# Kernel tuning notes

Measured on AMD Instinct MI355X. Metric: run time of the kernel, lower is better.

Reference implementation:

```python
import jax, jax.numpy as jnp
import numpy as np

N = 4096      # num_nodes (single graph; batch is all-zeros in the original when absent)
CIN = 1024    # in_channels
H = 1024      # hidden_channels
COUT = 512    # out_channels
R = 10        # nodevec rank (hardcoded in the module)
BN_EPS = 1e-5


def setup_inputs() -> dict:
    key = jax.random.key(0)
    ks = jax.random.split(key, 8)
    w = lambda k, shp: jax.random.normal(k, shp, dtype=jnp.float32) * 0.02
    return {
        "x": jax.random.normal(ks[0], (N, CIN), dtype=jnp.float32),
        "w_map": w(ks[1], (CIN, H)),
        "b_map": jnp.zeros((H,), jnp.float32),
        "nv1": jax.random.normal(ks[2], (N, R), dtype=jnp.float32),
        "nv2": jax.random.normal(ks[3], (R, N), dtype=jnp.float32),
        "w1": w(ks[4], (H, H)),
        "b1": jnp.zeros((H,), jnp.float32),
        "w2": w(ks[5], (H, COUT)),
        "b2": jnp.zeros((COUT,), jnp.float32),
        "bn1_g": jnp.ones((H,), jnp.float32),
        "bn1_b": jnp.zeros((H,), jnp.float32),
        "bn1_m": jnp.zeros((H,), jnp.float32),
        "bn1_v": jnp.ones((H,), jnp.float32),
        "bn2_g": jnp.ones((COUT,), jnp.float32),
        "bn2_b": jnp.zeros((COUT,), jnp.float32),
        "bn2_m": jnp.zeros((COUT,), jnp.float32),
        "bn2_v": jnp.ones((COUT,), jnp.float32),
        "w_attn": w(ks[6], (COUT, 1)),
        "b_attn": jnp.zeros((1,), jnp.float32),
    }


def _batchnorm_eval(h, g, b, m, v):
    # BatchNorm1d in eval mode: running stats
    return (h - m) * jax.lax.rsqrt(v + BN_EPS) * g + b


def reference(x, w_map, b_map, nv1, nv2, w1, b1, w2, b2,
              bn1_g, bn1_b, bn1_m, bn1_v, bn2_g, bn2_b, bn2_m, bn2_v,
              w_attn, b_attn):
    # feature mapping
    xm = jax.nn.relu(x @ w_map + b_map)                       # [N, H]
    # adaptive adjacency: softmax(relu(nv1 @ nv2), dim=1) -> strictly positive,
    # so nonzero() yields the fully dense edge list; we keep it dense.
    adp = jax.nn.softmax(jax.nn.relu(nv1 @ nv2), axis=1)      # [N, N]
    # gcn_norm (PyG GCNConv default): add unit self-loops, normalize by
    # column-degree^-1/2 on both sides.
    A = adp + jnp.eye(N, dtype=adp.dtype)                      # [N, N]
    deg = jnp.sum(A, axis=0)                                   # column sums (target degree)
    dinv = jnp.where(deg > 0, jax.lax.rsqrt(deg), 0.0)
    An = (dinv[:, None] * A) * dinv[None, :]                   # D^-1/2 A D^-1/2
    # GCNConv: out_i = sum_j An[j, i] * (x W)_j + bias  =>  An^T @ (X W) + b
    h = jax.nn.relu(An.T @ (xm @ w1) + b1)                     # conv1 + relu
    h = _batchnorm_eval(h, bn1_g, bn1_b, bn1_m, bn1_v)         # bn1 (dropout off in eval)
    h = jax.nn.relu(An.T @ (h @ w2) + b2)                      # conv2 + relu
    h = _batchnorm_eval(h, bn2_g, bn2_b, bn2_m, bn2_v)         # bn2
    # global_mean_pool with batch == zeros -> single-graph mean
    pooled = jnp.mean(h, axis=0, keepdims=True)                # [1, COUT]
    attn = jax.nn.sigmoid(pooled @ w_attn + b_attn)            # [1, 1]
    return pooled * attn                                       # [1, COUT]
```

## Files before the change

kernel.cpp:

```cpp
#include <hip/hip_runtime.h>

#define NN 4096
#define R_RANK 10

typedef __bf16 bf16x8 __attribute__((ext_vector_type(8)));
typedef float floatx4 __attribute__((ext_vector_type(4)));

__device__ __forceinline__ unsigned short f2bf(float f) {
    union { float f; unsigned int u; } v; v.f = f;
    unsigned int r = v.u + 0x7FFFu + ((v.u >> 16) & 1u);
    return (unsigned short)(r >> 16);
}
__device__ __forceinline__ void gll16(const void* g, void* l) {
    __builtin_amdgcn_global_load_lds(
        (const __attribute__((address_space(1))) unsigned int*)g,
        (__attribute__((address_space(3))) unsigned int*)l, 16, 0, 0);
}
template<int N>
__device__ __forceinline__ void wait_vm() {
    if constexpr (N == 0)      asm volatile("s_waitcnt vmcnt(0)" ::: "memory");
    else if constexpr (N == 6) asm volatile("s_waitcnt vmcnt(6)" ::: "memory");
    else if constexpr (N == 8) asm volatile("s_waitcnt vmcnt(8)" ::: "memory");
    else static_assert(N == 0 || N == 6 || N == 8, "add vmcnt literal");
}

__global__ __launch_bounds__(256) void row_stats_kernel(
    const float* __restrict__ nv1, const float* __restrict__ nv2,
    float* __restrict__ rowmax, float* __restrict__ rowsum,
    float* __restrict__ deg, float* __restrict__ pooled)
{
    const int i0 = blockIdx.x * 4;
    const int tid = threadIdx.x;
    if (blockIdx.x < 16) deg[blockIdx.x * 256 + tid] = 0.f;
    if (blockIdx.x >= 16 && blockIdx.x < 18) pooled[(blockIdx.x - 16) * 256 + tid] = 0.f;
    __shared__ float a[4][R_RANK];
    if (tid < 4 * R_RANK) a[tid / R_RANK][tid % R_RANK] = nv1[i0 * R_RANK + tid];
    __syncthreads();

    float s[4][16];
    float mx[4] = {0.f, 0.f, 0.f, 0.f};
    #pragma unroll
    for (int t = 0; t < 16; ++t) {
        const int j = t * 256 + tid;
        float v[R_RANK];
        #pragma unroll
        for (int r = 0; r < R_RANK; ++r) v[r] = nv2[r * NN + j];
        #pragma unroll
        for (int q = 0; q < 4; ++q) {
            float acc = 0.f;
            #pragma unroll
            for (int r = 0; r < R_RANK; ++r) acc = fmaf(a[q][r], v[r], acc);
            acc = fmaxf(acc, 0.f);
            s[q][t] = acc;
            mx[q] = fmaxf(mx[q], acc);
        }
    }
    __shared__ float red[4][4];
    #pragma unroll
    for (int q = 0; q < 4; ++q) {
        float m = mx[q];
        #pragma unroll
        for (int off = 32; off > 0; off >>= 1) m = fmaxf(m, __shfl_down(m, off, 64));
        if ((tid & 63) == 0) red[q][tid >> 6] = m;
    }
    __syncthreads();
    #pragma unroll
    for (int q = 0; q < 4; ++q)
        mx[q] = fmaxf(fmaxf(red[q][0], red[q][1]), fmaxf(red[q][2], red[q][3]));
    __syncthreads();
    float sm[4] = {0.f, 0.f, 0.f, 0.f};
    #pragma unroll
    for (int t = 0; t < 16; ++t)
        #pragma unroll
        for (int q = 0; q < 4; ++q) sm[q] += __expf(s[q][t] - mx[q]);
    #pragma unroll
    for (int q = 0; q < 4; ++q) {
        float m = sm[q];
        #pragma unroll
        for (int off = 32; off > 0; off >>= 1) m += __shfl_down(m, off, 64);
        if ((tid & 63) == 0) red[q][tid >> 6] = m;
    }
    __syncthreads();
    if (tid < 4) {
        rowmax[i0 + tid] = mx[tid];
        rowsum[i0 + tid] = red[tid][0] + red[tid][1] + red[tid][2] + red[tid][3];
    }
}

__global__ __launch_bounds__(256) void col_sum_kernel(
    const float* __restrict__ nv1, const float* __restrict__ nv2,
    const float* __restrict__ rowmax, const float* __restrict__ rowsum,
    float* __restrict__ deg)
{
    const int tid = threadIdx.x;
    const int j = blockIdx.x * 256 + tid;
    const int i0 = blockIdx.y * 64;
    __shared__ float a[64][R_RANK];
    __shared__ float rm[64], rs[64];
    if (tid < 64) {
        rm[tid] = rowmax[i0 + tid];
        rs[tid] = 1.0f / rowsum[i0 + tid];
    }
    for (int t = tid; t < 64 * R_RANK; t += 256)
        a[t / R_RANK][t % R_RANK] = nv1[i0 * R_RANK + t];
    __syncthreads();

    float v[R_RANK];
    #pragma unroll
    for (int r = 0; r < R_RANK; ++r) v[r] = nv2[r * NN + j];
    float acc = 0.f;
    #pragma unroll 4
    for (int t = 0; t < 64; ++t) {
        float s = 0.f;
        #pragma unroll
        for (int r = 0; r < R_RANK; ++r) s = fmaf(a[t][r], v[r], s);
        s = fmaxf(s, 0.f);
        acc += __expf(s - rm[t]) * rs[t];
    }
    atomicAdd(&deg[j], acc);
}

__global__ __launch_bounds__(256) void an_build_kernel(
    const float* __restrict__ nv1, const float* __restrict__ nv2,
    const float* __restrict__ rowmax, const float* __restrict__ rowsum,
    const float* __restrict__ deg, unsigned short* __restrict__ AnT)
{
    const int tid = threadIdx.x;
    const int j = blockIdx.x * 256 + tid;
    const int i0 = blockIdx.y * 8;
    __shared__ float v2s[8][R_RANK];
    __shared__ float dis[8];
    if (tid < 8 * R_RANK) {
        const int r = tid / 8, t = tid % 8;
        v2s[t][r] = nv2[r * NN + i0 + t];
    }
    if (tid < 8) dis[tid] = rsqrtf(1.0f + deg[i0 + tid]);

    float a[R_RANK];
    #pragma unroll
    for (int r = 0; r < R_RANK; ++r) a[r] = nv1[j * R_RANK + r];
    const float rm = rowmax[j];
    const float rs = 1.0f / rowsum[j];
    const float dj = rsqrtf(1.0f + deg[j]);
    __syncthreads();

    #pragma unroll
    for (int t = 0; t < 8; ++t) {
        const int i = i0 + t;
        float s = 0.f;
        #pragma unroll
        for (int r = 0; r < R_RANK; ++r) s = fmaf(a[r], v2s[t][r], s);
        s = fmaxf(s, 0.f);
        const float adp = __expf(s - rm) * rs;
        const float val = (adp + ((i == j) ? 1.f : 0.f)) * dis[t] * dj;
        AnT[(size_t)i * NN + j] = f2bf(val);
    }
}

__global__ __launch_bounds__(256) void prep_kernel(
    const float* __restrict__ x, const float* __restrict__ w_map,
    const float* __restrict__ w1, const float* __restrict__ w2,
    unsigned short* __restrict__ xb, unsigned short* __restrict__ wmT,
    unsigned short* __restrict__ w1T, unsigned short* __restrict__ w2T)
{
    const int z = blockIdx.z;
    const int tid = threadIdx.x;
    if (z == 3) {
        const int b = blockIdx.x + blockIdx.y * 32;
        const size_t base = (size_t)b * 4096 + (size_t)tid * 16;
        #pragma unroll
        for (int i = 0; i < 2; ++i) {
            const float4 a0 = *(const float4*)(x + base + i * 8);
            const float4 a1 = *(const float4*)(x + base + i * 8 + 4);
            ushort4 p, q;
            p.x = f2bf(a0.x); p.y = f2bf(a0.y); p.z = f2bf(a0.z); p.w = f2bf(a0.w);
            q.x = f2bf(a1.x); q.y = f2bf(a1.y); q.z = f2bf(a1.z); q.w = f2bf(a1.w);
            *(ushort4*)(xb + base + i * 8) = p;
            *(ushort4*)(xb + base + i * 8 + 4) = q;
        }
        return;
    }
    const float* W = (z == 0) ? w_map : (z == 1) ? w1 : w2;
    unsigned short* WT = (z == 0) ? wmT : (z == 1) ? w1T : w2T;
    const int CN = (z == 2) ? 512 : 1024;
    if (blockIdx.x * 32 >= CN) return;
    __shared__ float s[32][33];
    const int tx = tid & 31, ty = tid >> 5;
    const int r0 = blockIdx.y * 32, c0 = blockIdx.x * 32;
    #pragma unroll
    for (int i = 0; i < 4; ++i)
        s[ty + 8 * i][tx] = W[(size_t)(r0 + ty + 8 * i) * CN + c0 + tx];
    __syncthreads();
    #pragma unroll
    for (int i = 0; i < 4; ++i)
        WT[(size_t)(c0 + ty + 8 * i) * 1024 + r0 + tx] = f2bf(s[tx][ty + 8 * i]);
}

template<int OUTM, int EPI, int SK>
__global__ __launch_bounds__(512) void gemm_mfma(
    const unsigned short* __restrict__ A, const unsigned short* __restrict__ Bt,
    void* __restrict__ Out, const int M, const int N, const int K,
    const float* __restrict__ bias, const float* __restrict__ gamma,
    const float* __restrict__ beta, const float* __restrict__ mean,
    const float* __restrict__ var)
{
    __shared__ __align__(16) unsigned short As[4][8192];
    __shared__ __align__(16) unsigned short Bs[4][8192];
    const int tid = threadIdx.x;
    const int l = tid & 63, w = tid >> 6;
    const int wy = w >> 2, wx = w & 3;
    const int lr = l & 15, lq = l >> 4;

    const int gx = gridDim.x, gy = gridDim.y;
    int lin = blockIdx.x + gx * (blockIdx.y + gy * blockIdx.z);
    const int q = (gx * gy * gridDim.z) >> 3;
    lin = (lin & 7) * q + (lin >> 3);
    const int bx = lin % gx;
    const int by = (lin / gx) % gy;
    const int bz = lin / (gx * gy);

    const int row0 = by * 128, col0 = bx * 128;
    const int Kc = K / SK;
    const int kb = bz * Kc;
    const int nt = Kc >> 6;

    const unsigned short* Ag0 = A + (size_t)(row0 + w * 16 + lr) * K + kb + lq * 8;
    const unsigned short* Bg0 = Bt + (size_t)(col0 + w * 16 + lr) * K + kb + lq * 8;

    floatx4 acc[4][2];
    #pragma unroll
    for (int i = 0; i < 4; ++i)
        #pragma unroll
        for (int j = 0; j < 2; ++j) acc[i][j] = (floatx4){0.f, 0.f, 0.f, 0.f};

    #define STAGE(b, t)                                                         \
    {                                                                           \
        char* Aw = (char*)As[b] + w * 1024;                                     \
        char* Bw = (char*)Bs[b] + w * 1024;                                     \
        const int kk = (t) * 64;                                                \
        gll16(Ag0 + kk,      Aw);                                               \
        gll16(Ag0 + kk + 32, Aw + 8192);                                        \
        gll16(Bg0 + kk,      Bw);                                               \
        gll16(Bg0 + kk + 32, Bw + 8192);                                        \
    }

    STAGE(0, 0)
    STAGE(1, 1)
    const int nt2 = nt - 2;
    for (int t = 0; t < nt; ++t) {
        if (t < nt2) {
            STAGE((t + 2) & 3, t + 2)
            wait_vm<8>();
        } else if (t == nt2) {
            asm volatile("s_waitcnt vmcnt(4)" ::: "memory");
        } else {
            wait_vm<0>();
        }
        __builtin_amdgcn_sched_barrier(0);
        __builtin_amdgcn_s_barrier();
        __builtin_amdgcn_sched_barrier(0);

        const char* Afr = (const char*)As[t & 3] + wy * 4096 + l * 16;
        const char* Bfr = (const char*)Bs[t & 3] + wx * 2048 + l * 16;
        #pragma unroll
        for (int h = 0; h < 2; ++h) {
            bf16x8 af[4], bf[2];
            #pragma unroll
            for (int i = 0; i < 4; ++i) af[i] = *(const bf16x8*)(Afr + h * 8192 + i * 1024);
            #pragma unroll
            for (int j = 0; j < 2; ++j) bf[j] = *(const bf16x8*)(Bfr + h * 8192 + j * 1024);
            #pragma unroll
            for (int mf = 0; mf < 4; ++mf)
                #pragma unroll
                for (int nf = 0; nf < 2; ++nf)
                    acc[mf][nf] = __builtin_amdgcn_mfma_f32_16x16x32_bf16(
                        af[mf], bf[nf], acc[mf][nf], 0, 0, 0);
        }
    }
    #undef STAGE

    const int gr0 = row0 + wy * 64 + lq * 4;
    const int gc0 = col0 + wx * 32 + lr;
    if constexpr (OUTM == 0) {
        float* Pz = (float*)Out + (size_t)bz * M * N;
        #pragma unroll
        for (int mf = 0; mf < 4; ++mf) {
            const int gr = gr0 + mf * 16;
            #pragma unroll
            for (int nf = 0; nf < 2; ++nf) {
                const int gc = gc0 + nf * 16;
                #pragma unroll
                for (int r = 0; r < 4; ++r)
                    Pz[(size_t)(gr + r) * N + gc] = acc[mf][nf][r];
            }
        }
    } else {
        unsigned short* O = (unsigned short*)Out;
        #pragma unroll
        for (int nf = 0; nf < 2; ++nf) {
            const int gc = gc0 + nf * 16;
            float bb = 0.f, sc = 1.f, sh = 0.f;
            if constexpr (EPI >= 1) bb = bias[gc];
            if constexpr (EPI == 2) {
                sc = gamma[gc] * rsqrtf(var[gc] + 1e-5f);
                sh = beta[gc] - mean[gc] * sc;
            }
            #pragma unroll
            for (int mf = 0; mf < 4; ++mf) {
                const int gr = gr0 + mf * 16;
                #pragma unroll
                for (int r = 0; r < 4; ++r) {
                    float xv = acc[mf][nf][r];
                    if constexpr (EPI >= 1) xv = fmaxf(xv + bb, 0.f);
                    if constexpr (EPI == 2) xv = fmaf(xv, sc, sh);
                    O[(size_t)(gr + r) * N + gc] = f2bf(xv);
                }
            }
        }
    }
}

template<int BM, int BN, int SK>
__global__ __launch_bounds__(512, 2) void gemm_big(
    const unsigned short* __restrict__ A, const unsigned short* __restrict__ Bt,
    float* __restrict__ P, const int M, const int N, const int K)
{
    constexpr int MR = BM / 32;
    constexpr int NRF = BN / 64;
    constexpr int LL = (BM + BN) / 64;
    __shared__ __align__(16) unsigned short L[2][(BM + BN) * 64];
    const int tid = threadIdx.x;
    const int l = tid & 63, w = tid >> 6;
    const int wy = w >> 2, wx = w & 3;
    const int lr = l & 15, lq = l >> 4;

    const int gx = gridDim.x, gy = gridDim.y;
    int lin = blockIdx.x + gx * (blockIdx.y + gy * blockIdx.z);
    const int q = (gx * gy * gridDim.z) >> 3;
    lin = (lin & 7) * q + (lin >> 3);
    const int bx = lin % gx;
    const int by = (lin / gx) % gy;
    const int bz = lin / (gx * gy);

    const int row0 = by * BM, col0 = bx * BN;
    const int Kc = K / SK, kb = bz * Kc;
    const int nt = Kc >> 6;

    const unsigned short* Ag = A + (size_t)(row0 + w * (BM / 8) + lr) * K + kb + lq * 8;
    const unsigned short* Bg = Bt + (size_t)(col0 + w * (BN / 8) + lr) * K + kb + lq * 8;

    floatx4 acc[MR][NRF];
    #pragma unroll
    for (int i = 0; i < MR; ++i)
        #pragma unroll
        for (int j = 0; j < NRF; ++j) acc[i][j] = (floatx4){0.f, 0.f, 0.f, 0.f};

    #define STAGEB(b, t)                                                        \
    {                                                                           \
        char* Ld = (char*)L[b];                                                 \
        const int kk = (t) * 64;                                                \
        _Pragma("unroll")                                                       \
        for (int h = 0; h < 2; ++h) {                                           \
            _Pragma("unroll")                                                   \
            for (int s = 0; s < BM / 128; ++s)                                  \
                gll16(Ag + (size_t)(s * 16) * K + kk + h * 32,                  \
                      Ld + (w * (BM / 128) + s) * 1024 + h * (BM * 64));        \
            _Pragma("unroll")                                                   \
            for (int s = 0; s < BN / 128; ++s)                                  \
                gll16(Bg + (size_t)(s * 16) * K + kk + h * 32,                  \
                      Ld + BM * 128 + (w * (BN / 128) + s) * 1024 + h * (BN * 64)); \
        }                                                                       \
    }

    STAGEB(0, 0)
    int cur = 0;
    for (int t = 0; t < nt; ++t) {
        if (t + 1 < nt) {
            STAGEB(cur ^ 1, t + 1)
            wait_vm<LL>();
        } else {
            wait_vm<0>();
        }
        __builtin_amdgcn_sched_barrier(0);
        __builtin_amdgcn_s_barrier();
        __builtin_amdgcn_sched_barrier(0);

        const char* Ab = (const char*)L[cur] + wy * (BM / 32) * 1024 + l * 16;
        const char* Bb = (const char*)L[cur] + BM * 128 + wx * (BN / 64) * 1024 + l * 16;
        #pragma unroll
        for (int h = 0; h < 2; ++h) {
            bf16x8 af[MR], bf[NRF];
            #pragma unroll
            for (int i = 0; i < MR; ++i) af[i] = *(const bf16x8*)(Ab + h * (BM * 64) + i * 1024);
            #pragma unroll
            for (int j = 0; j < NRF; ++j) bf[j] = *(const bf16x8*)(Bb + h * (BN * 64) + j * 1024);
            __builtin_amdgcn_s_setprio(1);
            #pragma unroll
            for (int mf = 0; mf < MR; ++mf)
                #pragma unroll
                for (int nf = 0; nf < NRF; ++nf)
                    acc[mf][nf] = __builtin_amdgcn_mfma_f32_16x16x32_bf16(
                        af[mf], bf[nf], acc[mf][nf], 0, 0, 0);
            __builtin_amdgcn_s_setprio(0);
        }
        __builtin_amdgcn_sched_barrier(0);
        __builtin_amdgcn_s_barrier();
        __builtin_amdgcn_sched_barrier(0);
        cur ^= 1;
    }
    #undef STAGEB

    float* Pz = P + (size_t)bz * M * N;
    const int gr0 = row0 + wy * (BM / 2) + lq * 4;
    const int gc0 = col0 + wx * (BN / 4) + lr;
    #pragma unroll
    for (int mf = 0; mf < MR; ++mf) {
        const int gr = gr0 + mf * 16;
        #pragma unroll
        for (int nf = 0; nf < NRF; ++nf) {
            const int gc = gc0 + nf * 16;
            #pragma unroll
            for (int r = 0; r < 4; ++r)
                Pz[(size_t)(gr + r) * N + gc] = acc[mf][nf][r];
        }
    }
}

template<int EPI, int S, int NC>
__global__ __launch_bounds__(256) void reduce_k(
    const float* __restrict__ P, unsigned short* __restrict__ out, const int MN,
    const float* __restrict__ bias, const float* __restrict__ gamma,
    const float* __restrict__ beta, const float* __restrict__ mean,
    const float* __restrict__ var)
{
    const int idx = blockIdx.x * 256 + threadIdx.x;
    const int n4 = MN >> 2;
    const float4* Pv = (const float4*)P;
    float4 v = Pv[idx];
    #pragma unroll
    for (int z = 1; z < S; ++z) {
        const float4 t = Pv[idx + (size_t)z * n4];
        v.x += t.x; v.y += t.y; v.z += t.z; v.w += t.w;
    }
    float vals[4] = {v.x, v.y, v.z, v.w};
    if constexpr (EPI >= 1) {
        const int c0 = (idx << 2) & (NC - 1);
        const float4 b4 = *(const float4*)(bias + c0);
        const float bb[4] = {b4.x, b4.y, b4.z, b4.w};
        float sc[4], sh[4];
        if constexpr (EPI == 2) {
            const float4 g4 = *(const float4*)(gamma + c0);
            const float4 e4 = *(const float4*)(beta + c0);
            const float4 m4 = *(const float4*)(mean + c0);
            const float4 v4 = *(const float4*)(var + c0);
            const float gg[4] = {g4.x, g4.y, g4.z, g4.w};
            const float ee[4] = {e4.x, e4.y, e4.z, e4.w};
            const float mm[4] = {m4.x, m4.y, m4.z, m4.w};
            const float vv[4] = {v4.x, v4.y, v4.z, v4.w};
            #pragma unroll
            for (int j = 0; j < 4; ++j) {
                sc[j] = gg[j] * rsqrtf(vv[j] + 1e-5f);
                sh[j] = ee[j] - mm[j] * sc[j];
            }
        }
        #pragma unroll
        for (int j = 0; j < 4; ++j) {
            float xv = fmaxf(vals[j] + bb[j], 0.f);
            if constexpr (EPI == 2) xv = fmaf(xv, sc[j], sh[j]);
            vals[j] = xv;
        }
    }
    ushort4 p;
    p.x = f2bf(vals[0]); p.y = f2bf(vals[1]); p.z = f2bf(vals[2]); p.w = f2bf(vals[3]);
    *(ushort4*)(out + ((size_t)idx << 2)) = p;
}

template<int S>
__global__ __launch_bounds__(256) void reduce_pool_kernel(
    const float* __restrict__ P, float* __restrict__ pooled,
    const float* __restrict__ bias, const float* __restrict__ gamma,
    const float* __restrict__ beta, const float* __restrict__ mean,
    const float* __restrict__ var)
{
    const int idx = blockIdx.x * 256 + threadIdx.x;
    const int row = blockIdx.x >> 2;
    constexpr int n4 = 512 * 4096 / 4;
    const float4* Pv = (const float4*)P;
    float4 v = Pv[idx];
    #pragma unroll
    for (int z = 1; z < S; ++z) {
        const float4 t = Pv[idx + (size_t)z * n4];
        v.x += t.x; v.y += t.y; v.z += t.z; v.w += t.w;
    }
    const float b0 = bias[row];
    const float sc = gamma[row] * rsqrtf(var[row] + 1e-5f);
    const float sh = beta[row] - mean[row] * sc;
    float s = 0.f;
    const float vals[4] = {v.x, v.y, v.z, v.w};
    #pragma unroll
    for (int j = 0; j < 4; ++j)
        s += fmaf(fmaxf(vals[j] + b0, 0.f), sc, sh);
    #pragma unroll
    for (int off = 32; off > 0; off >>= 1) s += __shfl_down(s, off, 64);
    __shared__ float red[4];
    if ((threadIdx.x & 63) == 0) red[threadIdx.x >> 6] = s;
    __syncthreads();
    if (threadIdx.x == 0)
        atomicAdd(&pooled[row], red[0] + red[1] + red[2] + red[3]);
}

__global__ __launch_bounds__(512) void finalize_kernel(
    const float* __restrict__ pooled, const float* __restrict__ w_attn,
    const float* __restrict__ b_attn, float* __restrict__ out)
{
    const int c = threadIdx.x;
    __shared__ float red[512];
    const float p = pooled[c] * (1.0f / 4096.0f);
    red[c] = p * w_attn[c];
    __syncthreads();
    for (int s = 256; s > 0; s >>= 1) {
        if (c < s) red[c] += red[c + s];
        __syncthreads();
    }
    const float attn = 1.0f / (1.0f + __expf(-(red[0] + b_attn[0])));
    out[c] = p * attn;
}

extern "C" void kernel_launch(void* const* d_in, const int* in_sizes, int n_in,
                              void* d_out, int out_size, void* d_ws, size_t ws_size,
                              hipStream_t stream) {
    const float* x      = (const float*)d_in[0];
    const float* w_map  = (const float*)d_in[1];
    const float* b_map  = (const float*)d_in[2];
    const float* nv1    = (const float*)d_in[3];
    const float* nv2    = (const float*)d_in[4];
    const float* w1     = (const float*)d_in[5];
    const float* b1     = (const float*)d_in[6];
    const float* w2     = (const float*)d_in[7];
    const float* b2     = (const float*)d_in[8];
    const float* bn1_g  = (const float*)d_in[9];
    const float* bn1_b  = (const float*)d_in[10];
    const float* bn1_m  = (const float*)d_in[11];
    const float* bn1_v  = (const float*)d_in[12];
    const float* bn2_g  = (const float*)d_in[13];
    const float* bn2_b  = (const float*)d_in[14];
    const float* bn2_m  = (const float*)d_in[15];
    const float* bn2_v  = (const float*)d_in[16];
    const float* w_attn = (const float*)d_in[17];
    const float* b_attn = (const float*)d_in[18];
    float* out = (float*)d_out;

    const size_t MB = 1024 * 1024;
    const bool big = ws_size >= 118 * MB;
    char* ws = (char*)d_ws;
    unsigned short* AnT = (unsigned short*)(ws);
    float*          P   = (float*)(ws + 32 * MB);
    char* B0 = big ? (ws + 96 * MB) : (ws + 64 * MB);
    unsigned short* xb  = (unsigned short*)(B0);
    unsigned short* t1T = (unsigned short*)(B0);
    unsigned short* t2T = (unsigned short*)(B0);
    unsigned short* xm  = (unsigned short*)(B0 + 8 * MB);
    unsigned short* h1  = (unsigned short*)(B0 + 8 * MB);
    unsigned short* wmT = (unsigned short*)(B0 + 16 * MB);
    unsigned short* w1T = (unsigned short*)(B0 + 18 * MB);
    unsigned short* w2T = (unsigned short*)(B0 + 20 * MB);
    float* deg    = (float*)(B0 + 21 * MB);
    float* rowmax = deg + 4096;
    float* rowsum = rowmax + 4096;
    float* pooled = rowsum + 4096;

    prep_kernel<<<dim3(32, 32, 4), 256, 0, stream>>>(x, w_map, w1, w2, xb, wmT, w1T, w2T);
    row_stats_kernel<<<1024, 256, 0, stream>>>(nv1, nv2, rowmax, rowsum, deg, pooled);
    col_sum_kernel<<<dim3(16, 64), 256, 0, stream>>>(nv1, nv2, rowmax, rowsum, deg);
    an_build_kernel<<<dim3(16, 512), 256, 0, stream>>>(nv1, nv2, rowmax, rowsum, deg, AnT);

    gemm_mfma<1, 1, 1><<<dim3(8, 32, 1), 512, 0, stream>>>(xb, wmT, xm,
        4096, 1024, 1024, b_map, nullptr, nullptr, nullptr, nullptr);
    gemm_mfma<1, 0, 1><<<dim3(32, 8, 1), 512, 0, stream>>>(w1T, xm, t1T,
        1024, 4096, 1024, nullptr, nullptr, nullptr, nullptr, nullptr);
    if (big) {
        gemm_big<256, 256, 4><<<dim3(4, 16, 4), 512, 0, stream>>>(AnT, t1T, P, 4096, 1024, 4096);
        reduce_k<2, 4, 1024><<<4096, 256, 0, stream>>>(P, h1, 4194304,
            b1, bn1_g, bn1_b, bn1_m, bn1_v);
    } else {
        gemm_big<256, 128, 2><<<dim3(8, 16, 2), 512, 0, stream>>>(AnT, t1T, P, 4096, 1024, 4096);
        reduce_k<2, 2, 1024><<<4096, 256, 0, stream>>>(P, h1, 4194304,
            b1, bn1_g, bn1_b, bn1_m, bn1_v);
    }
    gemm_mfma<0, 0, 2><<<dim3(32, 4, 2), 512, 0, stream>>>(w2T, h1, P,
        512, 4096, 1024, nullptr, nullptr, nullptr, nullptr, nullptr);
    reduce_k<0, 2, 1><<<2048, 256, 0, stream>>>(P, t2T, 2097152,
        nullptr, nullptr, nullptr, nullptr, nullptr);
    gemm_big<128, 256, 4><<<dim3(16, 4, 4), 512, 0, stream>>>(t2T, AnT, P, 512, 4096, 4096);
    reduce_pool_kernel<4><<<2048, 256, 0, stream>>>(
        P, pooled, b2, bn2_g, bn2_b, bn2_m, bn2_v);

    finalize_kernel<<<1, 512, 0, stream>>>(pooled, w_attn, b_attn, out);
}
```

Measured before the change: 300.2 us.

## Deepen GEMM load pipelines to three-ahead prefetch with four LDS stages

Both GEMM kernels now prefetch three K-tiles ahead into a four-slot LDS ring instead of two (or one) ahead. In the large GEMM the K-tile shrinks from 64 to 32 so four stages fit, and launch bounds drop to one block per CU. A trailing barrier is added to the first GEMM so the deeper prefetch cannot overwrite a buffer still being read. The aim is to hide global-load latency better, at the cost of more barriers per K and lower occupancy.

```diff
diff --git a/kernel.cpp b/kernel.cpp
--- a/kernel.cpp
+++ b/kernel.cpp
@@ -18,10 +18,14 @@
 }
 template<int N>
 __device__ __forceinline__ void wait_vm() {
-    if constexpr (N == 0)      asm volatile("s_waitcnt vmcnt(0)" ::: "memory");
-    else if constexpr (N == 6) asm volatile("s_waitcnt vmcnt(6)" ::: "memory");
-    else if constexpr (N == 8) asm volatile("s_waitcnt vmcnt(8)" ::: "memory");
-    else static_assert(N == 0 || N == 6 || N == 8, "add vmcnt literal");
+    if constexpr (N == 0)       asm volatile("s_waitcnt vmcnt(0)" ::: "memory");
+    else if constexpr (N == 3)  asm volatile("s_waitcnt vmcnt(3)" ::: "memory");
+    else if constexpr (N == 4)  asm volatile("s_waitcnt vmcnt(4)" ::: "memory");
+    else if constexpr (N == 6)  asm volatile("s_waitcnt vmcnt(6)" ::: "memory");
+    else if constexpr (N == 8)  asm volatile("s_waitcnt vmcnt(8)" ::: "memory");
+    else if constexpr (N == 9)  asm volatile("s_waitcnt vmcnt(9)" ::: "memory");
+    else if constexpr (N == 12) asm volatile("s_waitcnt vmcnt(12)" ::: "memory");
+    else static_assert(N < 0, "add vmcnt literal");
 }
 
 __global__ __launch_bounds__(256) void row_stats_kernel(
@@ -246,13 +250,15 @@
 
     STAGE(0, 0)
     STAGE(1, 1)
-    const int nt2 = nt - 2;
+    STAGE(2, 2)
     for (int t = 0; t < nt; ++t) {
-        if (t < nt2) {
-            STAGE((t + 2) & 3, t + 2)
+        if (t + 3 < nt) {
+            STAGE((t + 3) & 3, t + 3)
+            wait_vm<12>();
+        } else if (t + 2 < nt) {
             wait_vm<8>();
-        } else if (t == nt2) {
-            asm volatile("s_waitcnt vmcnt(4)" ::: "memory");
+        } else if (t + 1 < nt) {
+            wait_vm<4>();
         } else {
             wait_vm<0>();
         }
@@ -276,6 +282,9 @@
                     acc[mf][nf] = __builtin_amdgcn_mfma_f32_16x16x32_bf16(
                         af[mf], bf[nf], acc[mf][nf], 0, 0, 0);
         }
+        __builtin_amdgcn_sched_barrier(0);
+        __builtin_amdgcn_s_barrier();
+        __builtin_amdgcn_sched_barrier(0);
     }
     #undef STAGE
 
@@ -321,14 +330,15 @@
 }
 
 template<int BM, int BN, int SK>
-__global__ __launch_bounds__(512, 2) void gemm_big(
+__global__ __launch_bounds__(512, 1) void gemm_big(
     const unsigned short* __restrict__ A, const unsigned short* __restrict__ Bt,
     float* __restrict__ P, const int M, const int N, const int K)
 {
     constexpr int MR = BM / 32;
     constexpr int NRF = BN / 64;
-    constexpr int LL = (BM + BN) / 64;
-    __shared__ __align__(16) unsigned short L[2][(BM + BN) * 64];
+    constexpr int LPT = (BM + BN) / 128;
+    constexpr int ABYTES = BM * 64;
+    __shared__ __align__(16) unsigned short L[4][(BM + BN) * 32];
     const int tid = threadIdx.x;
     const int l = tid & 63, w = tid >> 6;
     const int wy = w >> 2, wx = w & 3;
@@ -344,7 +354,7 @@
 
     const int row0 = by * BM, col0 = bx * BN;
     const int Kc = K / SK, kb = bz * Kc;
-    const int nt = Kc >> 6;
+    const int nt = Kc >> 5;
 
     const unsigned short* Ag = A + (size_t)(row0 + w * (BM / 8) + lr) * K + kb + lq * 8;
     const unsigned short* Bg = Bt + (size_t)(col0 + w * (BN / 8) + lr) * K + kb + lq * 8;
@@ -358,26 +368,28 @@
     #define STAGEB(b, t)                                                        \
     {                                                                           \
         char* Ld = (char*)L[b];                                                 \
-        const int kk = (t) * 64;                                                \
+        const int kk = (t) * 32;                                                \
         _Pragma("unroll")                                                       \
-        for (int h = 0; h < 2; ++h) {                                           \
-            _Pragma("unroll")                                                   \
-            for (int s = 0; s < BM / 128; ++s)                                  \
-                gll16(Ag + (size_t)(s * 16) * K + kk + h * 32,                  \
-                      Ld + (w * (BM / 128) + s) * 1024 + h * (BM * 64));        \
-            _Pragma("unroll")                                                   \
-            for (int s = 0; s < BN / 128; ++s)                                  \
-                gll16(Bg + (size_t)(s * 16) * K + kk + h * 32,                  \
-                      Ld + BM * 128 + (w * (BN / 128) + s) * 1024 + h * (BN * 64)); \
-        }                                                                       \
+        for (int s = 0; s < BM / 128; ++s)                                      \
+            gll16(Ag + (size_t)(s * 16) * K + kk,                               \
+                  Ld + (w * (BM / 128) + s) * 1024);                            \
+        _Pragma("unroll")                                                       \
+        for (int s = 0; s < BN / 128; ++s)                                      \
+            gll16(Bg + (size_t)(s * 16) * K + kk,                               \
+                  Ld + ABYTES + (w * (BN / 128) + s) * 1024);                   \
     }
 
     STAGEB(0, 0)
-    int cur = 0;
+    STAGEB(1, 1)
+    STAGEB(2, 2)
     for (int t = 0; t < nt; ++t) {
-        if (t + 1 < nt) {
-            STAGEB(cur ^ 1, t + 1)
-            wait_vm<LL>();
+        if (t + 3 < nt) {
+            STAGEB((t + 3) & 3, t + 3)
+            wait_vm<3 * LPT>();
+        } else if (t + 2 < nt) {
+            wait_vm<2 * LPT>();
+        } else if (t + 1 < nt) {
+            wait_vm<LPT>();
         } else {
             wait_vm<0>();
         }
@@ -385,28 +397,24 @@
         __builtin_amdgcn_s_barrier();
         __builtin_amdgcn_sched_barrier(0);
 
-        const char* Ab = (const char*)L[cur] + wy * (BM / 32) * 1024 + l * 16;
-        const char* Bb = (const char*)L[cur] + BM * 128 + wx * (BN / 64) * 1024 + l * 16;
-        #pragma unroll
-        for (int h = 0; h < 2; ++h) {
-            bf16x8 af[MR], bf[NRF];
-            #pragma unroll
-            for (int i = 0; i < MR; ++i) af[i] = *(const bf16x8*)(Ab + h * (BM * 64) + i * 1024);
-            #pragma unroll
-            for (int j = 0; j < NRF; ++j) bf[j] = *(const bf16x8*)(Bb + h * (BN * 64) + j * 1024);
-            __builtin_amdgcn_s_setprio(1);
-            #pragma unroll
-            for (int mf = 0; mf < MR; ++mf)
-                #pragma unroll
-                for (int nf = 0; nf < NRF; ++nf)
-                    acc[mf][nf] = __builtin_amdgcn_mfma_f32_16x16x32_bf16(
-                        af[mf], bf[nf], acc[mf][nf], 0, 0, 0);
-            __builtin_amdgcn_s_setprio(0);
-        }
+        const char* Ab = (const char*)L[t & 3] + wy * (MR * 1024) + l * 16;
+        const char* Bb = (const char*)L[t & 3] + ABYTES + wx * (NRF * 1024) + l * 16;
+        bf16x8 af[MR], bf[NRF];
+        #pragma unroll
+        for (int i = 0; i < MR; ++i) af[i] = *(const bf16x8*)(Ab + i * 1024);
+        #pragma unroll
+        for (int j = 0; j < NRF; ++j) bf[j] = *(const bf16x8*)(Bb + j * 1024);
+        __builtin_amdgcn_s_setprio(1);
+        #pragma unroll
+        for (int mf = 0; mf < MR; ++mf)
+            #pragma unroll
+            for (int nf = 0; nf < NRF; ++nf)
+                acc[mf][nf] = __builtin_amdgcn_mfma_f32_16x16x32_bf16(
+                    af[mf], bf[nf], acc[mf][nf], 0, 0, 0);
+        __builtin_amdgcn_s_setprio(0);
         __builtin_amdgcn_sched_barrier(0);
         __builtin_amdgcn_s_barrier();
         __builtin_amdgcn_sched_barrier(0);
-        cur ^= 1;
     }
     #undef STAGEB
 
```

New measurement: 309.0 us. +2.9%, slower.
